# Performance work log

Measured on AMD Instinct MI355X. Metric: run time of the kernel, lower is better.

Reference implementation:

```python
import jax, jax.numpy as jnp
import numpy as np

N, D, E = 32768, 768, 8
F = 4 * D  # 3072


def setup_inputs() -> dict:
    key = jax.random.key(0)
    ks = jax.random.split(key, 8)
    scale = 0.02
    hidden_states = jax.random.normal(ks[0], (N, D), dtype=jnp.float32)
    Wg = jax.random.normal(ks[1], (E, D), dtype=jnp.float32) * scale  # gate, no bias
    W1 = jax.random.normal(ks[2], (E, F, D), dtype=jnp.float32) * scale
    b1 = jnp.zeros((E, F), dtype=jnp.float32)
    W2 = jax.random.normal(ks[3], (E, D, F), dtype=jnp.float32) * scale
    b2 = jnp.zeros((E, D), dtype=jnp.float32)
    W3 = jax.random.normal(ks[4], (E, 1, D), dtype=jnp.float32) * scale
    b3 = jnp.zeros((E, 1), dtype=jnp.float32)
    return {"hidden_states": hidden_states, "Wg": Wg, "W1": W1, "b1": b1,
            "W2": W2, "b2": b2, "W3": W3, "b3": b3, "top_k": 2}


def reference(hidden_states, Wg, W1, b1, W2, b2, W3, b3, top_k):
    x = hidden_states  # [N, D]
    logits = x @ Wg.T  # [N, E]
    probs = jax.nn.softmax(logits.astype(jnp.float32), axis=-1)
    w, _sel = jax.lax.top_k(probs, top_k)  # [N, k] (descending)
    w = (w / w.sum(axis=-1, keepdims=True)).astype(x.dtype)
    # FAITHFUL TO SOURCE BUG: expert used is the position index j (experts[j]),
    # not the selected expert id. So densely run experts 0..top_k-1 on all tokens.
    W1k, b1k = W1[:top_k], b1[:top_k]
    W2k, b2k = W2[:top_k], b2[:top_k]
    W3k, b3k = W3[:top_k], b3[:top_k]
    # dropout is identity in eval mode
    h = jax.nn.relu(jnp.einsum('nd,kfd->knf', x, W1k) + b1k[:, None, :])  # [k,N,F]
    o = x[None, :, :] + jnp.einsum('knf,kdf->knd', h, W2k) + b2k[:, None, :]  # residual, [k,N,D]
    s = jnp.einsum('knd,kod->kno', o, W3k) + b3k[:, None, :]  # [k,N,1]
    out = jnp.sum(jnp.swapaxes(w, 0, 1)[:, :, None] * s, axis=0)  # [N,1]
    return out
```

## Files before the change

### kernel.cpp

```cpp
#include <hip/hip_runtime.h>
#include <hip/hip_bf16.h>
#include <stdint.h>

#define N_TOK 32768
#define DDIM  768
#define FDIM  3072
#define NCOLS (2*FDIM)
#define BK    32
#define KTILES (DDIM/BK)
#define NTILES (NCOLS/128)

typedef __attribute__((ext_vector_type(8))) short bf16x8;
typedef __attribute__((ext_vector_type(4))) float f32x4;

__device__ __forceinline__ unsigned short f2bf(float f) {
  unsigned u = __builtin_bit_cast(unsigned, f);
  unsigned r = (u + 0x7fffu + ((u >> 16) & 1u)) >> 16;
  return (unsigned short)r;
}

__device__ __forceinline__ void gl_lds16(const void* g, void* l) {
  __builtin_amdgcn_global_load_lds(
      (const __attribute__((address_space(1))) unsigned int*)g,
      (__attribute__((address_space(3))) unsigned int*)l, 16, 0, 0);
}

__global__ __launch_bounds__(256) void cvt_kernel(const float* __restrict__ src,
                                                  unsigned short* __restrict__ dst) {
  size_t i = ((size_t)blockIdx.x * 256 + threadIdx.x) * 4;
  float4 f = *(const float4*)(src + i);
  ushort4 u;
  u.x = f2bf(f.x); u.y = f2bf(f.y); u.z = f2bf(f.z); u.w = f2bf(f.w);
  *(ushort4*)(dst + i) = u;
}

__global__ __launch_bounds__(256) void vcalc_kernel(const float* __restrict__ W2,
                                                    const float* __restrict__ W3,
                                                    float* __restrict__ v) {
  __shared__ float w3s[DDIM];
  int k  = blockIdx.x / (FDIM/256);
  int fb = blockIdx.x % (FDIM/256);
  for (int d = threadIdx.x; d < DDIM; d += 256) w3s[d] = W3[k*DDIM + d];
  __syncthreads();
  int f = fb*256 + threadIdx.x;
  const float* W2k = W2 + (size_t)k * DDIM * FDIM + f;
  float s = 0.f;
  #pragma unroll 8
  for (int d = 0; d < DDIM; ++d) s += W2k[(size_t)d*FDIM] * w3s[d];
  v[k*FDIM + f] = s;
}

__global__ __launch_bounds__(256) void ccalc_kernel(const float* __restrict__ b2,
                                                    const float* __restrict__ W3,
                                                    const float* __restrict__ b3,
                                                    float* __restrict__ cbuf) {
  __shared__ float red[256];
  for (int k = 0; k < 2; ++k) {
    float s = 0.f;
    for (int d = threadIdx.x; d < DDIM; d += 256) s += b2[k*DDIM+d] * W3[k*DDIM+d];
    red[threadIdx.x] = s;
    __syncthreads();
    for (int off = 128; off > 0; off >>= 1) {
      if (threadIdx.x < off) red[threadIdx.x] += red[threadIdx.x+off];
      __syncthreads();
    }
    if (threadIdx.x == 0) cbuf[k] = red[0] + b3[k];
    __syncthreads();
  }
}

__global__ __launch_bounds__(256) void gate_cvt_kernel(
    const float* __restrict__ x, const float* __restrict__ Wg,
    const float* __restrict__ W3, const float* __restrict__ cbuf,
    unsigned short* __restrict__ xbf,
    float* __restrict__ wgt, float* __restrict__ base) {
  int wid  = threadIdx.x >> 6;
  int lane = threadIdx.x & 63;
  int n = blockIdx.x * 4 + wid;
  const float* xr = x + (size_t)n * DDIM;
  float acc[8] = {0,0,0,0,0,0,0,0};
  float d30 = 0.f, d31 = 0.f;
  #pragma unroll
  for (int it = 0; it < DDIM/64; ++it) {
    int i = it*64 + lane;
    float xv = xr[i];
    xbf[(size_t)n*DDIM + i] = f2bf(xv);
    #pragma unroll
    for (int e = 0; e < 8; ++e) acc[e] += xv * Wg[e*DDIM + i];
    d30 += xv * W3[i];
    d31 += xv * W3[DDIM + i];
  }
  #pragma unroll
  for (int m = 1; m < 64; m <<= 1) {
    #pragma unroll
    for (int e = 0; e < 8; ++e) acc[e] += __shfl_xor(acc[e], m, 64);
    d30 += __shfl_xor(d30, m, 64);
    d31 += __shfl_xor(d31, m, 64);
  }
  if (lane == 0) {
    float l1 = acc[0]; int a1 = 0;
    #pragma unroll
    for (int e = 1; e < 8; ++e) if (acc[e] > l1) { l1 = acc[e]; a1 = e; }
    float l2 = -3.4e38f;
    #pragma unroll
    for (int e = 0; e < 8; ++e) if (e != a1 && acc[e] > l2) l2 = acc[e];
    float w0 = 1.f / (1.f + __expf(l2 - l1));
    float w1 = 1.f - w0;
    wgt[2*n]   = w0;
    wgt[2*n+1] = w1;
    base[n] = w0 * (d30 + cbuf[0]) + w1 * (d31 + cbuf[1]);
  }
}

__global__ __launch_bounds__(256) void gemm_kernel(
    const unsigned short* __restrict__ A,
    const unsigned short* __restrict__ B,
    const float* __restrict__ b1,
    const float* __restrict__ v,
    float* __restrict__ part) {
  __shared__ __align__(16) unsigned short As[128*BK];
  __shared__ __align__(16) unsigned short Bs[128*BK];
  __shared__ float red[256];

  const int tid  = threadIdx.x;
  const int lane = tid & 63, wid = tid >> 6;
  const int wr = wid >> 1, wc = wid & 1;
  const int q  = lane >> 4, cl = lane & 15;
  const int bn = blockIdx.x;
  const int bm = blockIdx.y;

  const int r0  = tid >> 2;
  const int kq0 = (tid & 3) ^ ((r0 >> 1) & 3);
  const int r1  = r0 + 64;
  const int kq1 = (tid & 3) ^ ((r1 >> 1) & 3);

  const unsigned short* Ab = A + (size_t)bm * 128 * DDIM;
  const unsigned short* Bb = B + (size_t)bn * 128 * DDIM;

  f32x4 zero = {0.f, 0.f, 0.f, 0.f};
  f32x4 acc[4][4];
  #pragma unroll
  for (int i = 0; i < 4; ++i)
    #pragma unroll
    for (int j = 0; j < 4; ++j) acc[i][j] = zero;

  int aoff[4], boff[4];
  #pragma unroll
  for (int i = 0; i < 4; ++i) {
    int ra = wr*64 + i*16 + cl;
    aoff[i] = (ra*4 + (q ^ ((ra>>1)&3))) * 16;
    int rb = wc*64 + i*16 + cl;
    boff[i] = (rb*4 + (q ^ ((rb>>1)&3))) * 16;
  }
  char* AsB = (char*)As;
  char* BsB = (char*)Bs;

  for (int kt = 0; kt < KTILES; ++kt) {
    int k0 = kt * BK;
    gl_lds16(Ab + (size_t)r0*DDIM + k0 + kq0*8, AsB + wid*1024);
    gl_lds16(Ab + (size_t)r1*DDIM + k0 + kq1*8, AsB + 4096 + wid*1024);
    gl_lds16(Bb + (size_t)r0*DDIM + k0 + kq0*8, BsB + wid*1024);
    gl_lds16(Bb + (size_t)r1*DDIM + k0 + kq1*8, BsB + 4096 + wid*1024);
    __syncthreads();
    bf16x8 af[4], bfr[4];
    #pragma unroll
    for (int i = 0; i < 4; ++i) {
      af[i]  = *(const bf16x8*)(AsB + aoff[i]);
      bfr[i] = *(const bf16x8*)(BsB + boff[i]);
    }
    #pragma unroll
    for (int i = 0; i < 4; ++i)
      #pragma unroll
      for (int j = 0; j < 4; ++j)
        acc[i][j] = __builtin_amdgcn_mfma_f32_16x16x32_bf16(af[i], bfr[j], acc[i][j], 0, 0, 0);
    __syncthreads();
  }

  float vv[4], bb[4];
  #pragma unroll
  for (int j = 0; j < 4; ++j) {
    int cg = bn*128 + wc*64 + j*16 + cl;
    vv[j] = v[cg];
    bb[j] = b1[cg];
  }
  #pragma unroll
  for (int i = 0; i < 4; ++i) {
    #pragma unroll
    for (int r = 0; r < 4; ++r) {
      float s = 0.f;
      #pragma unroll
      for (int j = 0; j < 4; ++j) {
        float val = acc[i][j][r] + bb[j];
        val = fmaxf(val, 0.f);
        s += val * vv[j];
      }
      #pragma unroll
      for (int m = 1; m < 16; m <<= 1) s += __shfl_xor(s, m, 64);
      if (cl == 0) red[(wr*64 + i*16 + q*4 + r)*2 + wc] = s;
    }
  }
  __syncthreads();
  if (tid < 128)
    part[(size_t)bn * N_TOK + bm*128 + tid] = red[tid*2] + red[tid*2+1];
}

__global__ __launch_bounds__(256) void final_kernel(const float* __restrict__ part,
                                                    const float* __restrict__ wgt,
                                                    const float* __restrict__ base,
                                                    float* __restrict__ out) {
  int n = blockIdx.x * 256 + threadIdx.x;
  float s0 = 0.f, s1 = 0.f;
  #pragma unroll
  for (int t = 0; t < 24; ++t) s0 += part[(size_t)t*N_TOK + n];
  #pragma unroll
  for (int t = 24; t < 48; ++t) s1 += part[(size_t)t*N_TOK + n];
  out[n] = base[n] + wgt[2*n]*s0 + wgt[2*n+1]*s1;
}

extern "C" void kernel_launch(void* const* d_in, const int* in_sizes, int n_in,
                              void* d_out, int out_size, void* d_ws, size_t ws_size,
                              hipStream_t stream) {
  const float* x  = (const float*)d_in[0];
  const float* Wg = (const float*)d_in[1];
  const float* W1 = (const float*)d_in[2];
  const float* b1 = (const float*)d_in[3];
  const float* W2 = (const float*)d_in[4];
  const float* b2 = (const float*)d_in[5];
  const float* W3 = (const float*)d_in[6];
  const float* b3 = (const float*)d_in[7];
  float* out = (float*)d_out;

  char* ws = (char*)d_ws;
  size_t off = 0;
  auto alloc = [&](size_t bytes) -> char* {
    char* p = ws + off;
    off += (bytes + 255) & ~(size_t)255;
    return p;
  };
  unsigned short* xbf  = (unsigned short*)alloc((size_t)N_TOK * DDIM * 2);
  unsigned short* w1bf = (unsigned short*)alloc((size_t)NCOLS * DDIM * 2);
  float* v    = (float*)alloc((size_t)NCOLS * 4);
  float* cbuf = (float*)alloc(64);
  float* wgt  = (float*)alloc((size_t)N_TOK * 2 * 4);
  float* base = (float*)alloc((size_t)N_TOK * 4);
  float* part = (float*)alloc((size_t)NTILES * N_TOK * 4);
  if (off > ws_size) return;

  cvt_kernel<<<(NCOLS*DDIM)/1024, 256, 0, stream>>>(W1, w1bf);
  vcalc_kernel<<<2*(FDIM/256), 256, 0, stream>>>(W2, W3, v);
  ccalc_kernel<<<1, 256, 0, stream>>>(b2, W3, b3, cbuf);
  gate_cvt_kernel<<<N_TOK/4, 256, 0, stream>>>(x, Wg, W3, cbuf, xbf, wgt, base);
  gemm_kernel<<<dim3(NTILES, N_TOK/128), 256, 0, stream>>>(xbf, w1bf, b1, v, part);
  final_kernel<<<N_TOK/256, 256, 0, stream>>>(part, wgt, base, out);
}
```

Before: 695.1 us.

## Split W2·W3 reduction over D chunks, merge ccalc, vectorize gate loads

```diff
diff --git a/kernel.cpp b/kernel.cpp
--- a/kernel.cpp
+++ b/kernel.cpp
@@ -9,6 +9,7 @@
 #define BK    32
 #define KTILES (DDIM/BK)
 #define NTILES (NCOLS/128)
+#define VD_CHUNK 96
 
 typedef __attribute__((ext_vector_type(8))) short bf16x8;
 typedef __attribute__((ext_vector_type(4))) float f32x4;
@@ -36,36 +37,43 @@
 
 __global__ __launch_bounds__(256) void vcalc_kernel(const float* __restrict__ W2,
                                                     const float* __restrict__ W3,
-                                                    float* __restrict__ v) {
-  __shared__ float w3s[DDIM];
-  int k  = blockIdx.x / (FDIM/256);
-  int fb = blockIdx.x % (FDIM/256);
-  for (int d = threadIdx.x; d < DDIM; d += 256) w3s[d] = W3[k*DDIM + d];
+                                                    float* __restrict__ vpart) {
+  __shared__ float w3s[VD_CHUNK];
+  int k  = blockIdx.x / 12;
+  int fb = blockIdx.x % 12;
+  int db = blockIdx.y;
+  if (threadIdx.x < VD_CHUNK) w3s[threadIdx.x] = W3[k*DDIM + db*VD_CHUNK + threadIdx.x];
   __syncthreads();
   int f = fb*256 + threadIdx.x;
-  const float* W2k = W2 + (size_t)k * DDIM * FDIM + f;
+  const float* W2k = W2 + (size_t)k*DDIM*FDIM + (size_t)db*VD_CHUNK*FDIM + f;
   float s = 0.f;
   #pragma unroll 8
-  for (int d = 0; d < DDIM; ++d) s += W2k[(size_t)d*FDIM] * w3s[d];
-  v[k*FDIM + f] = s;
-}
-
-__global__ __launch_bounds__(256) void ccalc_kernel(const float* __restrict__ b2,
-                                                    const float* __restrict__ W3,
-                                                    const float* __restrict__ b3,
-                                                    float* __restrict__ cbuf) {
-  __shared__ float red[256];
-  for (int k = 0; k < 2; ++k) {
-    float s = 0.f;
-    for (int d = threadIdx.x; d < DDIM; d += 256) s += b2[k*DDIM+d] * W3[k*DDIM+d];
-    red[threadIdx.x] = s;
-    __syncthreads();
-    for (int off = 128; off > 0; off >>= 1) {
-      if (threadIdx.x < off) red[threadIdx.x] += red[threadIdx.x+off];
-      __syncthreads();
-    }
-    if (threadIdx.x == 0) cbuf[k] = red[0] + b3[k];
-    __syncthreads();
+  for (int d = 0; d < VD_CHUNK; ++d) s += W2k[(size_t)d*FDIM] * w3s[d];
+  vpart[(size_t)db*NCOLS + k*FDIM + f] = s;
+}
+
+__global__ __launch_bounds__(256) void vfinal_kernel(const float* __restrict__ vpart,
+                                                     float* __restrict__ v,
+                                                     const float* __restrict__ b2,
+                                                     const float* __restrict__ W3,
+                                                     const float* __restrict__ b3,
+                                                     float* __restrict__ cbuf) {
+  int f = blockIdx.x*256 + threadIdx.x;
+  float s = 0.f;
+  #pragma unroll
+  for (int db = 0; db < 8; ++db) s += vpart[(size_t)db*NCOLS + f];
+  v[f] = s;
+  if (blockIdx.x == 0 && threadIdx.x < 128) {
+    int k = threadIdx.x >> 6, lane = threadIdx.x & 63;
+    float c = 0.f;
+    #pragma unroll
+    for (int it = 0; it < DDIM/64; ++it) {
+      int i = it*64 + lane;
+      c += b2[k*DDIM + i] * W3[k*DDIM + i];
+    }
+    #pragma unroll
+    for (int m = 1; m < 64; m <<= 1) c += __shfl_xor(c, m, 64);
+    if (lane == 0) cbuf[k] = c + b3[k];
   }
 }
 
@@ -77,18 +85,26 @@
   int wid  = threadIdx.x >> 6;
   int lane = threadIdx.x & 63;
   int n = blockIdx.x * 4 + wid;
-  const float* xr = x + (size_t)n * DDIM;
+  const float4* xr = (const float4*)(x + (size_t)n * DDIM);
+  ushort4* xw = (ushort4*)(xbf + (size_t)n * DDIM);
   float acc[8] = {0,0,0,0,0,0,0,0};
   float d30 = 0.f, d31 = 0.f;
   #pragma unroll
-  for (int it = 0; it < DDIM/64; ++it) {
+  for (int it = 0; it < DDIM/256; ++it) {
     int i = it*64 + lane;
-    float xv = xr[i];
-    xbf[(size_t)n*DDIM + i] = f2bf(xv);
-    #pragma unroll
-    for (int e = 0; e < 8; ++e) acc[e] += xv * Wg[e*DDIM + i];
-    d30 += xv * W3[i];
-    d31 += xv * W3[DDIM + i];
+    float4 xv = xr[i];
+    ushort4 u;
+    u.x = f2bf(xv.x); u.y = f2bf(xv.y); u.z = f2bf(xv.z); u.w = f2bf(xv.w);
+    xw[i] = u;
+    #pragma unroll
+    for (int e = 0; e < 8; ++e) {
+      float4 w = ((const float4*)(Wg + e*DDIM))[i];
+      acc[e] += xv.x*w.x + xv.y*w.y + xv.z*w.z + xv.w*w.w;
+    }
+    float4 wa = ((const float4*)W3)[i];
+    d30 += xv.x*wa.x + xv.y*wa.y + xv.z*wa.z + xv.w*wa.w;
+    float4 wb = ((const float4*)(W3 + DDIM))[i];
+    d31 += xv.x*wb.x + xv.y*wb.y + xv.z*wb.z + xv.w*wb.w;
   }
   #pragma unroll
   for (int m = 1; m < 64; m <<= 1) {
@@ -239,16 +255,17 @@
   };
   unsigned short* xbf  = (unsigned short*)alloc((size_t)N_TOK * DDIM * 2);
   unsigned short* w1bf = (unsigned short*)alloc((size_t)NCOLS * DDIM * 2);
-  float* v    = (float*)alloc((size_t)NCOLS * 4);
-  float* cbuf = (float*)alloc(64);
-  float* wgt  = (float*)alloc((size_t)N_TOK * 2 * 4);
-  float* base = (float*)alloc((size_t)N_TOK * 4);
-  float* part = (float*)alloc((size_t)NTILES * N_TOK * 4);
+  float* vpart = (float*)alloc((size_t)8 * NCOLS * 4);
+  float* v     = (float*)alloc((size_t)NCOLS * 4);
+  float* cbuf  = (float*)alloc(64);
+  float* wgt   = (float*)alloc((size_t)N_TOK * 2 * 4);
+  float* base  = (float*)alloc((size_t)N_TOK * 4);
+  float* part  = (float*)alloc((size_t)NTILES * N_TOK * 4);
   if (off > ws_size) return;
 
   cvt_kernel<<<(NCOLS*DDIM)/1024, 256, 0, stream>>>(W1, w1bf);
-  vcalc_kernel<<<2*(FDIM/256), 256, 0, stream>>>(W2, W3, v);
-  ccalc_kernel<<<1, 256, 0, stream>>>(b2, W3, b3, cbuf);
+  vcalc_kernel<<<dim3(24, 8), 256, 0, stream>>>(W2, W3, vpart);
+  vfinal_kernel<<<NCOLS/256, 256, 0, stream>>>(vpart, v, b2, W3, b3, cbuf);
   gate_cvt_kernel<<<N_TOK/4, 256, 0, stream>>>(x, Wg, W3, cbuf, xbf, wgt, base);
   gemm_kernel<<<dim3(NTILES, N_TOK/128), 256, 0, stream>>>(xbf, w1bf, b1, v, part);
   final_kernel<<<N_TOK/256, 256, 0, stream>>>(part, wgt, base, out);
```

Result: faster. 631.2 us (-9.2%).
